# Kernel optimization log

Hardware: AMD Instinct MI355X
Metric: run time of the kernel (lower is better)

## Reference

```python
import jax, jax.numpy as jnp
import numpy as np

B, N_Z, N_E, D = 16, 2048, 2048, 512

def setup_inputs() -> dict:
    key = jax.random.key(0)
    kz, ke, km = jax.random.split(key, 3)
    z = jax.random.normal(kz, (B, N_Z, D), dtype=jnp.float32)
    e = jax.random.normal(ke, (B, N_E, D), dtype=jnp.float32)
    M = jax.random.normal(km, (D, D), dtype=jnp.float32)  # init: normal(0, 1)
    return {"z": z, "e": e, "M": M}

def reference(z, e, M):
    # a = z @ M @ e^T : [B, Nz, Ne]
    zM = jnp.einsum('bnd,de->bne', z, M)
    a = jnp.einsum('bnd,bmd->bnm', zM, e)
    a = jax.nn.sigmoid(a)
    # softmax over dim=1 (the Nz axis), as in the torch code
    A = jax.nn.softmax(a, axis=1)
    # out = A @ e : [B, Nz, D]
    return jnp.einsum('bnm,bmd->bnd', A, e)
```

## Files before the change

kernel.cpp:

```cpp
#include <hip/hip_runtime.h>
#include <hip/hip_bf16.h>
#include <stdint.h>

#define BB 16
#define NZ 2048
#define NE 2048
#define DD 512

typedef unsigned short u16;
typedef __attribute__((ext_vector_type(8))) _Float16 f16x8;
typedef __attribute__((ext_vector_type(4))) float f32x4;

__device__ __forceinline__ u16 f2h(float f) {
  _Float16 h = (_Float16)f;
  return __builtin_bit_cast(u16, h);
}

__device__ __forceinline__ float h2f(u16 h) {
  return (float)__builtin_bit_cast(_Float16, h);
}

__device__ __forceinline__ void gload_lds16(const void* g, void* l) {
  auto gp = (const __attribute__((address_space(1))) uint32_t*)g;
  auto lp = (__attribute__((address_space(3))) uint32_t*)l;
  __builtin_amdgcn_global_load_lds(gp, lp, 16, 0, 0);
}

#define FENCE() asm volatile("" ::: "memory")
#define BARRIER() do { FENCE(); __builtin_amdgcn_s_barrier(); FENCE(); } while (0)
#define WAIT_LGKM0() asm volatile("s_waitcnt lgkmcnt(0)" ::: "memory")
#define WAIT_VM(n) asm volatile("s_waitcnt vmcnt(" #n ")" ::: "memory")

__global__ void k_cvt(const float* __restrict__ in, u16* __restrict__ out, int n4) {
  int i = blockIdx.x * blockDim.x + threadIdx.x;
  int stride = gridDim.x * blockDim.x;
  for (; i < n4; i += stride) {
    float4 v = ((const float4*)in)[i];
    ushort4 o;
    o.x = f2h(v.x); o.y = f2h(v.y); o.z = f2h(v.z); o.w = f2h(v.w);
    ((ushort4*)out)[i] = o;
  }
}

__global__ void k_mt(const float* __restrict__ M, u16* __restrict__ Mt) {
  __shared__ float t[32][33];
  int bx = blockIdx.x * 32;
  int by = blockIdx.y * 32;
  for (int r = 0; r < 32; r += 8)
    t[threadIdx.y + r][threadIdx.x] = M[(size_t)(by + threadIdx.y + r) * DD + bx + threadIdx.x];
  __syncthreads();
  for (int r = 0; r < 32; r += 8)
    Mt[(size_t)(bx + threadIdx.y + r) * DD + by + threadIdx.x] = f2h(t[threadIdx.x][threadIdx.y + r]);
}

__global__ void k_et(const u16* __restrict__ eH, const float* __restrict__ cs,
                     u16* __restrict__ eT) {
  __shared__ float t[32][33];
  int b = blockIdx.z;
  int m0 = blockIdx.y * 32, d0 = blockIdx.x * 32;
  const u16* eb = eH + (size_t)b * NE * DD;
  const float* csb = cs + (size_t)b * NE;
  for (int r = 0; r < 32; r += 8) {
    int m = m0 + threadIdx.y + r;
    t[threadIdx.y + r][threadIdx.x] =
        h2f(eb[(size_t)m * DD + d0 + threadIdx.x]) * (2048.0f / csb[m]);
  }
  __syncthreads();
  u16* eTb = eT + (size_t)b * DD * NE;
  for (int r = 0; r < 32; r += 8) {
    int d = d0 + threadIdx.y + r;
    eTb[(size_t)d * NE + m0 + threadIdx.x] = f2h(t[threadIdx.x][threadIdx.y + r]);
  }
}

template<int EPI, int KDIM>
__global__ __launch_bounds__(512, 2) void k_gemm(
    const u16* __restrict__ A, const u16* __restrict__ Bt, void* __restrict__ Cp,
    int Ndim, long long sAb, long long sBb, long long sCb,
    float* __restrict__ colsum, int csld)
{
  extern __shared__ char lds[];
  constexpr int NT = KDIM / 64;

  const int gx = gridDim.x, gy = gridDim.y;
  const int nwg = gx * gy * gridDim.z;
  const int hid = blockIdx.x + gx * (blockIdx.y + gy * blockIdx.z);
  const int logical = (hid & 7) * (nwg >> 3) + (hid >> 3);
  const int bx = logical % gx;
  const int rem0 = logical / gx;
  const int by = rem0 % gy;
  const int bz = rem0 / gy;

  const int tid = threadIdx.x;
  const int lane = tid & 63;
  const int wid = tid >> 6;
  const int wr = wid >> 2;
  const int wc = wid & 3;

  const int row0 = by * 256;
  const int col0 = bx * 256;

  const u16* Ab = A + (long long)bz * sAb;
  const u16* Bb = Bt + (long long)bz * sBb;

  const u16* srcA[4]; const u16* srcB[4];
#pragma unroll
  for (int c = 0; c < 4; ++c) {
    int idx = c * 512 + tid;
    int ks = idx >> 10, rm = idx & 1023;
    int mf = rm >> 6, q = (rm >> 4) & 3, p = rm & 15;
    int r = mf * 16 + p, c8 = ks * 4 + q;
    srcA[c] = Ab + (long long)(row0 + r) * KDIM + c8 * 8;
    srcB[c] = Bb + (long long)(col0 + r) * KDIM + c8 * 8;
  }

  auto stageA = [&](int buf, int k0, int c0) {
#pragma unroll
    for (int c = c0; c < c0 + 2; ++c)
      gload_lds16(srcA[c] + k0, lds + buf * 32768 + (c * 512 + wid * 64) * 16);
  };
  auto stageB = [&](int buf, int k0, int c0) {
#pragma unroll
    for (int c = c0; c < c0 + 2; ++c)
      gload_lds16(srcB[c] + k0, lds + 65536 + buf * 32768 + (c * 512 + wid * 64) * 16);
  };

  auto ldA = [&](int buf, int ks, int m) -> f16x8 {
    return *(const f16x8*)(lds + buf * 32768 +
                           ((ks * 16 + wr * 8 + m) * 64 + lane) * 16);
  };
  auto ldB = [&](int buf, int ks, int n) -> f16x8 {
    return *(const f16x8*)(lds + 65536 + buf * 32768 +
                           ((ks * 16 + wc * 4 + n) * 64 + lane) * 16);
  };

  f32x4 acc[8][4] = {};
  f16x8 af[4], bf[4];

  stageA(0, 0, 0); stageB(0, 0, 0);
  stageA(0, 0, 2); stageB(0, 0, 2);
  WAIT_VM(4);
  BARRIER();

  for (int t = 0; t < NT; ++t) {
    const int buf = t & 1;
    const bool pf = (t + 1 < NT);
    const int nk0 = (t + 1) * 64;
#pragma unroll
    for (int m = 0; m < 4; ++m) af[m] = ldA(buf, 0, m);
#pragma unroll
    for (int n = 0; n < 4; ++n) bf[n] = ldB(buf, 0, n);
    if (pf) stageA(buf ^ 1, nk0, 0);
    BARRIER();
    WAIT_LGKM0();
    __builtin_amdgcn_s_setprio(1);
#pragma unroll
    for (int m = 0; m < 4; ++m)
#pragma unroll
      for (int n = 0; n < 4; ++n)
        acc[m][n] = __builtin_amdgcn_mfma_f32_16x16x32_f16(af[m], bf[n], acc[m][n], 0, 0, 0);
    __builtin_amdgcn_s_setprio(0);
    BARRIER();
#pragma unroll
    for (int m = 0; m < 4; ++m) af[m] = ldA(buf, 0, 4 + m);
    if (pf) stageB(buf ^ 1, nk0, 0);
    BARRIER();
    WAIT_LGKM0();
    __builtin_amdgcn_s_setprio(1);
#pragma unroll
    for (int m = 0; m < 4; ++m)
#pragma unroll
      for (int n = 0; n < 4; ++n)
        acc[4 + m][n] = __builtin_amdgcn_mfma_f32_16x16x32_f16(af[m], bf[n], acc[4 + m][n], 0, 0, 0);
    __builtin_amdgcn_s_setprio(0);
    if (pf) { WAIT_VM(4); } else { WAIT_VM(0); }
    BARRIER();
#pragma unroll
    for (int m = 0; m < 4; ++m) af[m] = ldA(buf, 1, m);
#pragma unroll
    for (int n = 0; n < 4; ++n) bf[n] = ldB(buf, 1, n);
    if (pf) stageA(buf ^ 1, nk0, 2);
    BARRIER();
    WAIT_LGKM0();
    __builtin_amdgcn_s_setprio(1);
#pragma unroll
    for (int m = 0; m < 4; ++m)
#pragma unroll
      for (int n = 0; n < 4; ++n)
        acc[m][n] = __builtin_amdgcn_mfma_f32_16x16x32_f16(af[m], bf[n], acc[m][n], 0, 0, 0);
    __builtin_amdgcn_s_setprio(0);
    BARRIER();
#pragma unroll
    for (int m = 0; m < 4; ++m) af[m] = ldA(buf, 1, 4 + m);
    if (pf) stageB(buf ^ 1, nk0, 2);
    BARRIER();
    WAIT_LGKM0();
    __builtin_amdgcn_s_setprio(1);
#pragma unroll
    for (int m = 0; m < 4; ++m)
#pragma unroll
      for (int n = 0; n < 4; ++n)
        acc[4 + m][n] = __builtin_amdgcn_mfma_f32_16x16x32_f16(af[m], bf[n], acc[4 + m][n], 0, 0, 0);
    __builtin_amdgcn_s_setprio(0);
    if (pf) { WAIT_VM(4); }
    BARRIER();
  }

  const int rr = (lane >> 4) * 4;
  const int cc = lane & 15;
  if constexpr (EPI == 0) {
    u16* C = (u16*)Cp + (long long)bz * sCb;
#pragma unroll
    for (int m = 0; m < 8; ++m)
#pragma unroll
      for (int n = 0; n < 4; ++n)
#pragma unroll
        for (int j = 0; j < 4; ++j) {
          int row = row0 + wr * 128 + m * 16 + rr + j;
          int col = col0 + wc * 64 + n * 16 + cc;
          C[(long long)row * Ndim + col] = f2h(acc[m][n][j]);
        }
  } else if constexpr (EPI == 1) {
    u16* C = (u16*)Cp + (long long)bz * sCb;
    float csum[4] = {0.f, 0.f, 0.f, 0.f};
#pragma unroll
    for (int m = 0; m < 8; ++m)
#pragma unroll
      for (int n = 0; n < 4; ++n)
#pragma unroll
        for (int j = 0; j < 4; ++j) {
          float x = acc[m][n][j];
          float s = 1.f / (1.f + __expf(-x));
          float v = __expf(s);
          int row = row0 + wr * 128 + m * 16 + rr + j;
          int col = col0 + wc * 64 + n * 16 + cc;
          C[(long long)row * Ndim + col] = f2h(v);
          csum[n] += v;
        }
#pragma unroll
    for (int n = 0; n < 4; ++n) {
      float v = csum[n];
      v += __shfl_xor(v, 16, 64);
      v += __shfl_xor(v, 32, 64);
      if ((lane >> 4) == 0)
        atomicAdd(&colsum[(long long)bz * csld + col0 + wc * 64 + n * 16 + cc], v);
    }
  } else {
    float* C = (float*)Cp + (long long)bz * sCb;
#pragma unroll
    for (int m = 0; m < 8; ++m)
#pragma unroll
      for (int n = 0; n < 4; ++n)
#pragma unroll
        for (int j = 0; j < 4; ++j) {
          int row = row0 + wr * 128 + m * 16 + rr + j;
          int col = col0 + wc * 64 + n * 16 + cc;
          C[(long long)row * Ndim + col] = acc[m][n][j] * (1.0f / 2048.0f);
        }
  }
}

extern "C" void kernel_launch(void* const* d_in, const int* in_sizes, int n_in,
                              void* d_out, int out_size, void* d_ws, size_t ws_size,
                              hipStream_t stream) {
  const float* z = (const float*)d_in[0];
  const float* e = (const float*)d_in[1];
  const float* M = (const float*)d_in[2];
  float* out = (float*)d_out;
  char* ws = (char*)d_ws;

  u16* S    = (u16*)(ws + 0LL);
  u16* zM   = (u16*)(ws + 134217728LL);
  u16* zH   = (u16*)(ws + 167772160LL);
  u16* eH   = (u16*)(ws + 201326592LL);
  u16* Mt   = (u16*)(ws + 234881024LL);
  float* cs = (float*)(ws + 235405312LL);

  (void)hipFuncSetAttribute(reinterpret_cast<const void*>(&k_gemm<0, 512>),
                            hipFuncAttributeMaxDynamicSharedMemorySize, 131072);
  (void)hipFuncSetAttribute(reinterpret_cast<const void*>(&k_gemm<1, 512>),
                            hipFuncAttributeMaxDynamicSharedMemorySize, 131072);
  (void)hipFuncSetAttribute(reinterpret_cast<const void*>(&k_gemm<2, 2048>),
                            hipFuncAttributeMaxDynamicSharedMemorySize, 131072);

  hipMemsetAsync(cs, 0, (size_t)BB * NE * sizeof(float), stream);

  k_cvt<<<4096, 256, 0, stream>>>(z, zH, BB * NZ * DD / 4);
  k_cvt<<<4096, 256, 0, stream>>>(e, eH, BB * NE * DD / 4);
  k_mt<<<dim3(16, 16), dim3(32, 8), 0, stream>>>(M, Mt);

  k_gemm<0, 512><<<dim3(DD / 256, (BB * NZ) / 256, 1), 512, 131072, stream>>>(
      zH, Mt, zM, DD, 0LL, 0LL, 0LL, nullptr, 0);

  k_gemm<1, 512><<<dim3(NE / 256, NZ / 256, BB), 512, 131072, stream>>>(
      zM, eH, S, NE,
      (long long)NZ * DD, (long long)NE * DD, (long long)NZ * NE, cs, NE);

  u16* eT = zH;
  k_et<<<dim3(DD / 32, NE / 32, BB), dim3(32, 8), 0, stream>>>(eH, cs, eT);

  k_gemm<2, 2048><<<dim3(DD / 256, NZ / 256, BB), 512, 131072, stream>>>(
      S, eT, out, DD,
      (long long)NZ * NE, (long long)DD * NE, (long long)NZ * DD, nullptr, 0);
}
```

Before: 279.8 us.

## Simplify GEMM main loop to bulk prefetch with two barriers per tile

Replaces the finely interleaved four-phase K-tile loop with a simpler schedule. All eight global-to-LDS prefetch loads for the next tile are issued at the start of each iteration. Then two K-substeps each load 8 A and 4 B fragments and run all 32 MFMAs, relying on vmcnt waits to order the two halves. This removes about six barriers, the explicit lgkmcnt waits and the setprio toggles per iteration, cutting synchronisation overhead. In exchange it raises fragment register pressure and loses the fine-grained overlap of LDS reads with MFMA between waves.

```diff
diff --git a/kernel.cpp b/kernel.cpp
--- a/kernel.cpp
+++ b/kernel.cpp
@@ -28,7 +28,6 @@
 
 #define FENCE() asm volatile("" ::: "memory")
 #define BARRIER() do { FENCE(); __builtin_amdgcn_s_barrier(); FENCE(); } while (0)
-#define WAIT_LGKM0() asm volatile("s_waitcnt lgkmcnt(0)" ::: "memory")
 #define WAIT_VM(n) asm volatile("s_waitcnt vmcnt(" #n ")" ::: "memory")
 
 __global__ void k_cvt(const float* __restrict__ in, u16* __restrict__ out, int n4) {
@@ -114,96 +113,69 @@
     srcB[c] = Bb + (long long)(col0 + r) * KDIM + c8 * 8;
   }
 
-  auto stageA = [&](int buf, int k0, int c0) {
-#pragma unroll
-    for (int c = c0; c < c0 + 2; ++c)
-      gload_lds16(srcA[c] + k0, lds + buf * 32768 + (c * 512 + wid * 64) * 16);
+  auto stage = [&](char* dA, char* dB, int k0) {
+#pragma unroll
+    for (int c = 0; c < 2; ++c) {
+      gload_lds16(srcA[c] + k0, dA + (c * 512 + wid * 64) * 16);
+      gload_lds16(srcB[c] + k0, dB + (c * 512 + wid * 64) * 16);
+    }
+#pragma unroll
+    for (int c = 2; c < 4; ++c) {
+      gload_lds16(srcA[c] + k0, dA + (c * 512 + wid * 64) * 16);
+      gload_lds16(srcB[c] + k0, dB + (c * 512 + wid * 64) * 16);
+    }
   };
-  auto stageB = [&](int buf, int k0, int c0) {
-#pragma unroll
-    for (int c = c0; c < c0 + 2; ++c)
-      gload_lds16(srcB[c] + k0, lds + 65536 + buf * 32768 + (c * 512 + wid * 64) * 16);
-  };
-
-  auto ldA = [&](int buf, int ks, int m) -> f16x8 {
-    return *(const f16x8*)(lds + buf * 32768 +
-                           ((ks * 16 + wr * 8 + m) * 64 + lane) * 16);
-  };
-  auto ldB = [&](int buf, int ks, int n) -> f16x8 {
-    return *(const f16x8*)(lds + 65536 + buf * 32768 +
-                           ((ks * 16 + wc * 4 + n) * 64 + lane) * 16);
-  };
 
   f32x4 acc[8][4] = {};
-  f16x8 af[4], bf[4];
-
-  stageA(0, 0, 0); stageB(0, 0, 0);
-  stageA(0, 0, 2); stageB(0, 0, 2);
+
+  stage(lds, lds + 65536, 0);
   WAIT_VM(4);
   BARRIER();
 
   for (int t = 0; t < NT; ++t) {
     const int buf = t & 1;
+    char* lA = lds + buf * 32768;
+    char* lB = lds + 65536 + buf * 32768;
     const bool pf = (t + 1 < NT);
-    const int nk0 = (t + 1) * 64;
-#pragma unroll
-    for (int m = 0; m < 4; ++m) af[m] = ldA(buf, 0, m);
-#pragma unroll
-    for (int n = 0; n < 4; ++n) bf[n] = ldB(buf, 0, n);
-    if (pf) stageA(buf ^ 1, nk0, 0);
+
+    if (pf) stage(lds + (buf ^ 1) * 32768, lds + 65536 + (buf ^ 1) * 32768,
+                  (t + 1) * 64);
+
+    {
+      f16x8 af[8], bf[4];
+#pragma unroll
+      for (int m = 0; m < 8; ++m)
+        af[m] = *(const f16x8*)(lA + ((0 * 16 + wr * 8 + m) * 64 + lane) * 16);
+#pragma unroll
+      for (int n = 0; n < 4; ++n)
+        bf[n] = *(const f16x8*)(lB + ((0 * 16 + wc * 4 + n) * 64 + lane) * 16);
+#pragma unroll
+      for (int m = 0; m < 8; ++m)
+#pragma unroll
+        for (int n = 0; n < 4; ++n)
+          acc[m][n] = __builtin_amdgcn_mfma_f32_16x16x32_f16(af[m], bf[n], acc[m][n], 0, 0, 0);
+    }
+    if (pf) { WAIT_VM(8); } else { WAIT_VM(0); }
     BARRIER();
-    WAIT_LGKM0();
-    __builtin_amdgcn_s_setprio(1);
-#pragma unroll
-    for (int m = 0; m < 4; ++m)
-#pragma unroll
-      for (int n = 0; n < 4; ++n)
-        acc[m][n] = __builtin_amdgcn_mfma_f32_16x16x32_f16(af[m], bf[n], acc[m][n], 0, 0, 0);
-    __builtin_amdgcn_s_setprio(0);
-    BARRIER();
-#pragma unroll
-    for (int m = 0; m < 4; ++m) af[m] = ldA(buf, 0, 4 + m);
-    if (pf) stageB(buf ^ 1, nk0, 0);
-    BARRIER();
-    WAIT_LGKM0();
-    __builtin_amdgcn_s_setprio(1);
-#pragma unroll
-    for (int m = 0; m < 4; ++m)
-#pragma unroll
-      for (int n = 0; n < 4; ++n)
-        acc[4 + m][n] = __builtin_amdgcn_mfma_f32_16x16x32_f16(af[m], bf[n], acc[4 + m][n], 0, 0, 0);
-    __builtin_amdgcn_s_setprio(0);
-    if (pf) { WAIT_VM(4); } else { WAIT_VM(0); }
-    BARRIER();
-#pragma unroll
-    for (int m = 0; m < 4; ++m) af[m] = ldA(buf, 1, m);
-#pragma unroll
-    for (int n = 0; n < 4; ++n) bf[n] = ldB(buf, 1, n);
-    if (pf) stageA(buf ^ 1, nk0, 2);
-    BARRIER();
-    WAIT_LGKM0();
-    __builtin_amdgcn_s_setprio(1);
-#pragma unroll
-    for (int m = 0; m < 4; ++m)
-#pragma unroll
-      for (int n = 0; n < 4; ++n)
-        acc[m][n] = __builtin_amdgcn_mfma_f32_16x16x32_f16(af[m], bf[n], acc[m][n], 0, 0, 0);
-    __builtin_amdgcn_s_setprio(0);
-    BARRIER();
-#pragma unroll
-    for (int m = 0; m < 4; ++m) af[m] = ldA(buf, 1, 4 + m);
-    if (pf) stageB(buf ^ 1, nk0, 2);
-    BARRIER();
-    WAIT_LGKM0();
-    __builtin_amdgcn_s_setprio(1);
-#pragma unroll
-    for (int m = 0; m < 4; ++m)
-#pragma unroll
-      for (int n = 0; n < 4; ++n)
-        acc[4 + m][n] = __builtin_amdgcn_mfma_f32_16x16x32_f16(af[m], bf[n], acc[4 + m][n], 0, 0, 0);
-    __builtin_amdgcn_s_setprio(0);
-    if (pf) { WAIT_VM(4); }
-    BARRIER();
+
+    {
+      f16x8 af[8], bf[4];
+#pragma unroll
+      for (int m = 0; m < 8; ++m)
+        af[m] = *(const f16x8*)(lA + ((1 * 16 + wr * 8 + m) * 64 + lane) * 16);
+#pragma unroll
+      for (int n = 0; n < 4; ++n)
+        bf[n] = *(const f16x8*)(lB + ((1 * 16 + wc * 4 + n) * 64 + lane) * 16);
+#pragma unroll
+      for (int m = 0; m < 8; ++m)
+#pragma unroll
+        for (int n = 0; n < 4; ++n)
+          acc[m][n] = __builtin_amdgcn_mfma_f32_16x16x32_f16(af[m], bf[n], acc[m][n], 0, 0, 0);
+    }
+    if (pf) {
+      WAIT_VM(4);
+      BARRIER();
+    }
   }
 
   const int rr = (lane >> 4) * 4;
```

After: 285.7 us. 1.02x slower.
